# Performance work log

Measured on AMD Instinct MI355X. Metric: run time of the kernel, lower is better.

The kernel has to match this reference:

```python
import jax, jax.numpy as jnp
import numpy as np

B, S, D, H = 4, 2048, 1024, 16
HD = D // H  # head dim = 64


def setup_inputs() -> dict:
    key = jax.random.key(0)
    ks = jax.random.split(key, 6)
    hidden_states = jax.random.normal(ks[0], (B, S, D), dtype=jnp.float32)
    attention_mask = jnp.zeros((B, S), dtype=bool)  # ignored by the module (set to None in forward)
    # RoPE cache: standard rotary angles per position
    inv_freq = 1.0 / (10000.0 ** (jnp.arange(0, HD, 2, dtype=jnp.float32) / HD))  # [HD/2]
    ang = jnp.arange(S, dtype=jnp.float32)[:, None] * inv_freq[None, :]  # [S, HD/2]
    ang = jnp.concatenate([ang, ang], axis=-1)  # [S, HD]
    rope_cos = jnp.cos(ang)
    rope_sin = jnp.sin(ang)
    scale = 1.0 / np.sqrt(D)
    Wq = jax.random.normal(ks[1], (D, D), dtype=jnp.float32) * scale
    Wk = jax.random.normal(ks[2], (D, D), dtype=jnp.float32) * scale
    Wv = jax.random.normal(ks[3], (D, D), dtype=jnp.float32) * scale
    return {"hidden_states": hidden_states, "attention_mask": attention_mask,
            "rope_cos": rope_cos, "rope_sin": rope_sin, "Wq": Wq, "Wk": Wk, "Wv": Wv}


def _rotate_half(x):
    x1, x2 = jnp.split(x, 2, axis=-1)
    return jnp.concatenate([-x2, x1], axis=-1)


def _apply_rope(x, cos, sin):
    # x: [B, H, S, HD]; cos/sin: [S, HD]
    return x * cos[None, None, :, :] + _rotate_half(x) * sin[None, None, :, :]


def reference(hidden_states, attention_mask, rope_cos, rope_sin, Wq, Wk, Wv):
    del attention_mask  # forward() sets attention_mask = None
    b, s, d = hidden_states.shape
    # QKV projections (nn.Linear: y = x @ W.T), split into heads -> [B, H, S, HD]
    def proj(W):
        y = jnp.einsum('bsd,ed->bse', hidden_states, W)
        return y.reshape(b, s, H, HD).transpose(0, 2, 1, 3)
    q = _apply_rope(proj(Wq), rope_cos, rope_sin)
    k = _apply_rope(proj(Wk), rope_cos, rope_sin)
    v = proj(Wv)
    # Softmax attention (non-causal, dropout_p=0)
    scores = jnp.einsum('bhqd,bhkd->bhqk', q, k) / np.sqrt(HD)
    probs = jax.nn.softmax(scores, axis=-1)
    ctx = jnp.einsum('bhqk,bhkd->bhqd', probs, v)
    # [B, H, S, HD] -> [B, S, D]
    return ctx.transpose(0, 2, 1, 3).reshape(b, s, d)
```

## Files before the change

kernel.cpp:

```cpp
#include <hip/hip_runtime.h>
#include <hip/hip_bf16.h>
#include <stdint.h>


typedef __attribute__((ext_vector_type(4))) float    f32x4;
typedef __attribute__((ext_vector_type(8))) __bf16   bf16x8;
typedef __attribute__((ext_vector_type(8))) unsigned short ushort8;
typedef __attribute__((ext_vector_type(4))) unsigned short ushort4v;

#define QSCALE 0.18033688011112042f
#define SMAX   16.0f

#define GL16(g, l)                                                            \
  __builtin_amdgcn_global_load_lds(                                           \
      (const __attribute__((address_space(1))) void*)(g),                     \
      (__attribute__((address_space(3))) void*)(l), 16, 0, 0)

__device__ inline unsigned short bf(float f) {
  return __builtin_bit_cast(unsigned short, (__bf16)f);
}

__global__ __launch_bounds__(256) void cvt_bf16(
    const float* __restrict__ X,
    const float* __restrict__ Wq, const float* __restrict__ Wk,
    const float* __restrict__ Wv,
    unsigned short* __restrict__ Xb, unsigned short* __restrict__ Wb)
{
  const int seg = blockIdx.y;
  const float* __restrict__ src = (seg == 0) ? X : (seg == 1) ? Wq : (seg == 2) ? Wk : Wv;
  unsigned short* __restrict__ dst = (seg == 0) ? Xb : Wb + (size_t)(seg - 1) * 1048576;
  const size_t n8 = (seg == 0) ? (size_t)1048576 : (size_t)131072;
  const size_t stride = (size_t)gridDim.x * 256;
  for (size_t i = blockIdx.x * 256 + threadIdx.x; i < n8; i += stride) {
    const float4 a = *reinterpret_cast<const float4*>(src + i * 8);
    const float4 b = *reinterpret_cast<const float4*>(src + i * 8 + 4);
    ushort8 o = { bf(a.x), bf(a.y), bf(a.z), bf(a.w), bf(b.x), bf(b.y), bf(b.z), bf(b.w) };
    *reinterpret_cast<ushort8*>(dst + i * 8) = o;
  }
}

__global__ __launch_bounds__(256) void qkv_gemm(
    const unsigned short* __restrict__ Xb, const unsigned short* __restrict__ Wb,
    const float* __restrict__ rc, const float* __restrict__ rs,
    unsigned short* __restrict__ Qb, unsigned short* __restrict__ Kb,
    unsigned short* __restrict__ VbT, int col0, int nheads_c, int gx)
{
  const int nwg = gridDim.x;
  const int q8 = nwg >> 3;
  int w = (blockIdx.x % 8) * q8 + blockIdx.x / 8;
  const int z = w / (gx * 64);
  const int r = w - z * gx * 64;
  const int brow = (r / gx) * 128;
  const int bcol = (r % gx) * 128;

  const unsigned short* __restrict__ Wz = Wb + (size_t)z * 1048576;

  const int tid  = threadIdx.x;
  const int lane = tid & 63;
  const int wid  = tid >> 6;
  const int wm = wid >> 1, wn = wid & 1;
  const int col16 = lane & 15, rowg = lane >> 4;

  __shared__ unsigned short As[128 * 32];
  __shared__ unsigned short Bs[128 * 32];

  f32x4 acc[4][4];
  #pragma unroll
  for (int m = 0; m < 4; ++m)
    #pragma unroll
    for (int n = 0; n < 4; ++n) acc[m][n] = (f32x4)0.f;

  const int srow = wid * 16 + (lane >> 2);
  const int scol = (lane & 3) * 8;
  const unsigned short* gA0 = Xb + (size_t)(brow + srow) * 1024 + scol;
  const unsigned short* gA1 = gA0 + (size_t)64 * 1024;
  const unsigned short* gB0 = Wz + (size_t)(col0 + bcol + srow) * 1024 + scol;
  const unsigned short* gB1 = gB0 + (size_t)64 * 1024;
  unsigned short* lA0 = &As[wid * 16 * 32];
  unsigned short* lA1 = &As[(64 + wid * 16) * 32];
  unsigned short* lB0 = &Bs[wid * 16 * 32];
  unsigned short* lB1 = &Bs[(64 + wid * 16) * 32];

  for (int k0 = 0; k0 < 1024; k0 += 32) {
    GL16(gA0 + k0, lA0);
    GL16(gA1 + k0, lA1);
    GL16(gB0 + k0, lB0);
    GL16(gB1 + k0, lB1);
    __syncthreads();

    bf16x8 af[4], bfv[4];
    #pragma unroll
    for (int m = 0; m < 4; ++m)
      af[m] = __builtin_bit_cast(bf16x8, *reinterpret_cast<const ushort8*>(
                &As[(wm * 64 + m * 16 + col16) * 32 + rowg * 8]));
    #pragma unroll
    for (int n = 0; n < 4; ++n)
      bfv[n] = __builtin_bit_cast(bf16x8, *reinterpret_cast<const ushort8*>(
                &Bs[(wn * 64 + n * 16 + col16) * 32 + rowg * 8]));
    #pragma unroll
    for (int m = 0; m < 4; ++m)
      #pragma unroll
      for (int n = 0; n < 4; ++n)
        acc[m][n] = __builtin_amdgcn_mfma_f32_16x16x32_bf16(af[m], bfv[n], acc[m][n], 0, 0, 0);
    __syncthreads();
  }

  #pragma unroll
  for (int m = 0; m < 4; ++m) {
    #pragma unroll
    for (int n = 0; n < 4; ++n) {
      const int e  = bcol + wn * 64 + n * 16 + col16;
      const int hl = e >> 6, hd = e & 63;
      if (z == 2) {
        const int row0 = brow + wm * 64 + m * 16 + rowg * 4;
        const int b = row0 >> 11, s0 = row0 & 2047;
        ushort4v o = { bf(acc[m][n][0]), bf(acc[m][n][1]), bf(acc[m][n][2]), bf(acc[m][n][3]) };
        *reinterpret_cast<ushort4v*>(
            VbT + ((size_t)(b * nheads_c + hl) * 64 + hd) * 2048 + s0) = o;
      } else {
        unsigned short* __restrict__ outp = (z == 0) ? Qb : Kb;
        #pragma unroll
        for (int j = 0; j < 4; ++j) {
          const int row = brow + wm * 64 + m * 16 + rowg * 4 + j;
          const int b = row >> 11, s = row & 2047;
          const float rot = (n < 2) ? -acc[m][n + 2][j] : acc[m][n - 2][j];
          float v = acc[m][n][j] * rc[s * 64 + hd] + rot * rs[s * 64 + hd];
          if (z == 0) v *= QSCALE;
          outp[((size_t)(b * nheads_c + hl) * 2048 + s) * 64 + hd] = bf(v);
        }
      }
    }
  }
}

__global__ __launch_bounds__(512) void attn(
    const unsigned short* __restrict__ Qb, const unsigned short* __restrict__ Kb,
    const unsigned short* __restrict__ VbT, float* __restrict__ out,
    int col0, int nheads_c)
{
  const int tid = threadIdx.x, lane = tid & 63, wq = tid >> 6;
  const int col16 = lane & 15, rowg = lane >> 4;

  int wg = blockIdx.x;
  const int qx = (int)gridDim.x >> 3;
  wg = (wg & 7) * qx + (wg >> 3);
  const int bh = wg >> 4;
  const int q0 = (wg & 15) * 128;
  const int b = bh / nheads_c, hl = bh - b * nheads_c;
  const int hg = (col0 >> 6) + hl;
  const size_t base = (size_t)bh * 2048 * 64;

  __shared__ unsigned short Ks[64 * 72];
  __shared__ unsigned short Vt[64 * 72];
  __shared__ unsigned short Ps[128 * 76];

  const int sr = tid >> 3, sc8 = (tid & 7) * 8;

  #pragma unroll
  for (int p = 0; p < 2; ++p) {
    const int row = p * 64 + sr;
    ushort8 v = *reinterpret_cast<const ushort8*>(Qb + base + (size_t)(q0 + row) * 64 + sc8);
    *reinterpret_cast<ushort8*>(&Ps[row * 76 + sc8]) = v;
  }
  __syncthreads();
  bf16x8 qf[2];
  #pragma unroll
  for (int ks = 0; ks < 2; ++ks)
    qf[ks] = __builtin_bit_cast(bf16x8, *reinterpret_cast<const ushort8*>(
        &Ps[(wq * 16 + col16) * 76 + ks * 32 + rowg * 8]));

  float lsum[4] = {0.f, 0.f, 0.f, 0.f};
  f32x4 acc[4];
  #pragma unroll
  for (int hf = 0; hf < 4; ++hf) acc[hf] = (f32x4)0.f;

  for (int kt = 0; kt < 32; ++kt) {
    const int key0 = kt * 64;
    {
      ushort8 kv = *reinterpret_cast<const ushort8*>(Kb + base + (size_t)(key0 + sr) * 64 + sc8);
      ushort8 vv = *reinterpret_cast<const ushort8*>(VbT + base + (size_t)sr * 2048 + key0 + sc8);
      *reinterpret_cast<ushort8*>(&Ks[sr * 72 + sc8]) = kv;
      *reinterpret_cast<ushort8*>(&Vt[sr * 72 + sc8]) = vv;
    }
    __syncthreads();

    f32x4 sc[4];
    #pragma unroll
    for (int kf = 0; kf < 4; ++kf) sc[kf] = (f32x4)0.f;
    #pragma unroll
    for (int kf = 0; kf < 4; ++kf) {
      #pragma unroll
      for (int ks = 0; ks < 2; ++ks) {
        bf16x8 kfrag = __builtin_bit_cast(bf16x8, *reinterpret_cast<const ushort8*>(
            &Ks[(kf * 16 + col16) * 72 + ks * 32 + rowg * 8]));
        sc[kf] = __builtin_amdgcn_mfma_f32_16x16x32_bf16(qf[ks], kfrag, sc[kf], 0, 0, 0);
      }
    }

    #pragma unroll
    for (int j = 0; j < 4; ++j) {
      float ps = 0.f;
      #pragma unroll
      for (int kf = 0; kf < 4; ++kf) {
        const float p = __builtin_exp2f(sc[kf][j] - SMAX);
        sc[kf][j] = p;
        ps += p;
      }
      lsum[j] += ps;
    }

    #pragma unroll
    for (int kf = 0; kf < 4; ++kf)
      #pragma unroll
      for (int j = 0; j < 4; ++j)
        Ps[(wq * 16 + rowg * 4 + j) * 76 + kf * 16 + col16] = bf(sc[kf][j]);
    __syncthreads();

    #pragma unroll
    for (int ks = 0; ks < 2; ++ks) {
      bf16x8 pf = __builtin_bit_cast(bf16x8, *reinterpret_cast<const ushort8*>(
          &Ps[(wq * 16 + col16) * 76 + ks * 32 + rowg * 8]));
      #pragma unroll
      for (int hf = 0; hf < 4; ++hf) {
        bf16x8 vf = __builtin_bit_cast(bf16x8, *reinterpret_cast<const ushort8*>(
            &Vt[(hf * 16 + col16) * 72 + ks * 32 + rowg * 8]));
        acc[hf] = __builtin_amdgcn_mfma_f32_16x16x32_bf16(pf, vf, acc[hf], 0, 0, 0);
      }
    }
    __syncthreads();
  }

  #pragma unroll
  for (int j = 0; j < 4; ++j) {
    float l = lsum[j];
    l += __shfl_xor(l, 1);
    l += __shfl_xor(l, 2);
    l += __shfl_xor(l, 4);
    l += __shfl_xor(l, 8);
    const float inv = 1.0f / l;
    const int s = q0 + wq * 16 + rowg * 4 + j;
    #pragma unroll
    for (int hf = 0; hf < 4; ++hf) {
      const int hd = hf * 16 + col16;
      out[((size_t)(b * 2048 + s)) * 1024 + hg * 64 + hd] = acc[hf][j] * inv;
    }
  }
}

extern "C" void kernel_launch(void* const* d_in, const int* in_sizes, int n_in,
                              void* d_out, int out_size, void* d_ws, size_t ws_size,
                              hipStream_t stream) {
  (void)in_sizes; (void)n_in; (void)out_size;
  const float* X  = (const float*)d_in[0];
  const float* rc = (const float*)d_in[2];
  const float* rs = (const float*)d_in[3];
  const float* Wq = (const float*)d_in[4];
  const float* Wk = (const float*)d_in[5];
  const float* Wv = (const float*)d_in[6];
  float* out = (float*)d_out;

  const size_t fixed = (size_t)2 * 8192 * 1024 + (size_t)3 * 2 * 1024 * 1024;
  int NC = 8;
  for (int nc = 1; nc <= 8; nc <<= 1) {
    size_t need = (size_t)3 * 2 * 8192 * (1024 / nc) + fixed;
    if (need <= ws_size) { NC = nc; break; }
  }
  const int CW = 1024 / NC;
  const int nheads_c = CW >> 6;
  const int nBH = 4 * nheads_c;
  const int gx = CW / 128;
  const size_t pc = (size_t)8192 * CW;

  unsigned short* Qb  = (unsigned short*)d_ws;
  unsigned short* Kb  = Qb + pc;
  unsigned short* VbT = Kb + pc;
  unsigned short* Xb  = VbT + pc;
  unsigned short* Wb  = Xb + (size_t)8192 * 1024;

  cvt_bf16<<<dim3(512, 4), 256, 0, stream>>>(X, Wq, Wk, Wv, Xb, Wb);

  for (int c = 0; c < NC; ++c) {
    const int col0 = c * CW;
    qkv_gemm<<<dim3(gx * 64 * 3), 256, 0, stream>>>(
        Xb, Wb, rc, rs, Qb, Kb, VbT, col0, nheads_c, gx);
    attn<<<dim3(16 * nBH), 512, 0, stream>>>(
        Qb, Kb, VbT, out, col0, nheads_c);
  }
}
```

Baseline: 220.2 us.

## Keep softmax probabilities in registers using 32x32 MFMA and permlane swap

The attention kernel now uses 32x32x16 bf16 MFMAs with 4 waves of 256 threads, each covering 32 query rows. It computes the score tile transposed (keys by queries) so the exponentiated probabilities can be packed to bf16 with v_cvt_pk_bf16_f32. They are then rearranged into PV operand layout with permlane32_swap instead of being written to and read back from shared memory. This removes the Ps LDS buffer and one barrier per key tile, and Q fragments are loaded straight from global memory. In exchange each wave holds larger accumulators, which raises register pressure, and row sums pass through a small shared array for the final normalisation.

```diff
diff --git a/kernel.cpp b/kernel.cpp
--- a/kernel.cpp
+++ b/kernel.cpp
@@ -3,10 +3,13 @@
 #include <stdint.h>
 
 
-typedef __attribute__((ext_vector_type(4))) float    f32x4;
-typedef __attribute__((ext_vector_type(8))) __bf16   bf16x8;
-typedef __attribute__((ext_vector_type(8))) unsigned short ushort8;
-typedef __attribute__((ext_vector_type(4))) unsigned short ushort4v;
+typedef __attribute__((ext_vector_type(4)))  float    f32x4;
+typedef __attribute__((ext_vector_type(16))) float    f32x16;
+typedef __attribute__((ext_vector_type(8)))  __bf16   bf16x8;
+typedef __attribute__((ext_vector_type(8)))  unsigned short ushort8;
+typedef __attribute__((ext_vector_type(4)))  unsigned short ushort4v;
+typedef __attribute__((ext_vector_type(4)))  uint32_t uint32x4;
+typedef __attribute__((ext_vector_type(2)))  uint32_t uint32x2;
 
 #define QSCALE 0.18033688011112042f
 #define SMAX   16.0f
@@ -18,6 +21,11 @@
 
 __device__ inline unsigned short bf(float f) {
   return __builtin_bit_cast(unsigned short, (__bf16)f);
+}
+__device__ inline uint32_t cvtpk(float lo, float hi) {
+  uint32_t r;
+  asm volatile("v_cvt_pk_bf16_f32 %0, %1, %2" : "=v"(r) : "v"(lo), "v"(hi));
+  return r;
 }
 
 __global__ __launch_bounds__(256) void cvt_bf16(
@@ -133,13 +141,13 @@
   }
 }
 
-__global__ __launch_bounds__(512) void attn(
+__global__ __launch_bounds__(256) void attn(
     const unsigned short* __restrict__ Qb, const unsigned short* __restrict__ Kb,
     const unsigned short* __restrict__ VbT, float* __restrict__ out,
     int col0, int nheads_c)
 {
   const int tid = threadIdx.x, lane = tid & 63, wq = tid >> 6;
-  const int col16 = lane & 15, rowg = lane >> 4;
+  const int l31 = lane & 31, hi = lane >> 5;
 
   int wg = blockIdx.x;
   const int qx = (int)gridDim.x >> 3;
@@ -152,98 +160,85 @@
 
   __shared__ unsigned short Ks[64 * 72];
   __shared__ unsigned short Vt[64 * 72];
-  __shared__ unsigned short Ps[128 * 76];
+  __shared__ float Ls[4 * 32];
+
+  const int qrow = q0 + wq * 32 + l31;
+  bf16x8 qf[4];
+  #pragma unroll
+  for (int ds = 0; ds < 4; ++ds)
+    qf[ds] = __builtin_bit_cast(bf16x8, *reinterpret_cast<const ushort8*>(
+        Qb + base + (size_t)qrow * 64 + ds * 16 + hi * 8));
+
+  f32x16 acc0 = (f32x16)0.f, acc1 = (f32x16)0.f;
+  float ps = 0.f;
 
   const int sr = tid >> 3, sc8 = (tid & 7) * 8;
-
-  #pragma unroll
-  for (int p = 0; p < 2; ++p) {
-    const int row = p * 64 + sr;
-    ushort8 v = *reinterpret_cast<const ushort8*>(Qb + base + (size_t)(q0 + row) * 64 + sc8);
-    *reinterpret_cast<ushort8*>(&Ps[row * 76 + sc8]) = v;
-  }
-  __syncthreads();
-  bf16x8 qf[2];
-  #pragma unroll
-  for (int ks = 0; ks < 2; ++ks)
-    qf[ks] = __builtin_bit_cast(bf16x8, *reinterpret_cast<const ushort8*>(
-        &Ps[(wq * 16 + col16) * 76 + ks * 32 + rowg * 8]));
-
-  float lsum[4] = {0.f, 0.f, 0.f, 0.f};
-  f32x4 acc[4];
-  #pragma unroll
-  for (int hf = 0; hf < 4; ++hf) acc[hf] = (f32x4)0.f;
 
   for (int kt = 0; kt < 32; ++kt) {
     const int key0 = kt * 64;
     {
-      ushort8 kv = *reinterpret_cast<const ushort8*>(Kb + base + (size_t)(key0 + sr) * 64 + sc8);
-      ushort8 vv = *reinterpret_cast<const ushort8*>(VbT + base + (size_t)sr * 2048 + key0 + sc8);
-      *reinterpret_cast<ushort8*>(&Ks[sr * 72 + sc8]) = kv;
-      *reinterpret_cast<ushort8*>(&Vt[sr * 72 + sc8]) = vv;
-    }
-    __syncthreads();
-
-    f32x4 sc[4];
-    #pragma unroll
-    for (int kf = 0; kf < 4; ++kf) sc[kf] = (f32x4)0.f;
-    #pragma unroll
-    for (int kf = 0; kf < 4; ++kf) {
-      #pragma unroll
-      for (int ks = 0; ks < 2; ++ks) {
-        bf16x8 kfrag = __builtin_bit_cast(bf16x8, *reinterpret_cast<const ushort8*>(
-            &Ks[(kf * 16 + col16) * 72 + ks * 32 + rowg * 8]));
-        sc[kf] = __builtin_amdgcn_mfma_f32_16x16x32_bf16(qf[ks], kfrag, sc[kf], 0, 0, 0);
-      }
-    }
-
-    #pragma unroll
-    for (int j = 0; j < 4; ++j) {
-      float ps = 0.f;
-      #pragma unroll
-      for (int kf = 0; kf < 4; ++kf) {
-        const float p = __builtin_exp2f(sc[kf][j] - SMAX);
-        sc[kf][j] = p;
-        ps += p;
-      }
-      lsum[j] += ps;
-    }
-
-    #pragma unroll
-    for (int kf = 0; kf < 4; ++kf)
-      #pragma unroll
-      for (int j = 0; j < 4; ++j)
-        Ps[(wq * 16 + rowg * 4 + j) * 76 + kf * 16 + col16] = bf(sc[kf][j]);
-    __syncthreads();
-
-    #pragma unroll
-    for (int ks = 0; ks < 2; ++ks) {
-      bf16x8 pf = __builtin_bit_cast(bf16x8, *reinterpret_cast<const ushort8*>(
-          &Ps[(wq * 16 + col16) * 76 + ks * 32 + rowg * 8]));
-      #pragma unroll
-      for (int hf = 0; hf < 4; ++hf) {
-        bf16x8 vf = __builtin_bit_cast(bf16x8, *reinterpret_cast<const ushort8*>(
-            &Vt[(hf * 16 + col16) * 72 + ks * 32 + rowg * 8]));
-        acc[hf] = __builtin_amdgcn_mfma_f32_16x16x32_bf16(pf, vf, acc[hf], 0, 0, 0);
-      }
-    }
-    __syncthreads();
-  }
-
-  #pragma unroll
-  for (int j = 0; j < 4; ++j) {
-    float l = lsum[j];
-    l += __shfl_xor(l, 1);
-    l += __shfl_xor(l, 2);
-    l += __shfl_xor(l, 4);
-    l += __shfl_xor(l, 8);
-    const float inv = 1.0f / l;
-    const int s = q0 + wq * 16 + rowg * 4 + j;
-    #pragma unroll
-    for (int hf = 0; hf < 4; ++hf) {
-      const int hd = hf * 16 + col16;
-      out[((size_t)(b * 2048 + s)) * 1024 + hg * 64 + hd] = acc[hf][j] * inv;
-    }
+      ushort8 k0v = *reinterpret_cast<const ushort8*>(Kb + base + (size_t)(key0 + sr) * 64 + sc8);
+      ushort8 k1v = *reinterpret_cast<const ushort8*>(Kb + base + (size_t)(key0 + 32 + sr) * 64 + sc8);
+      ushort8 v0v = *reinterpret_cast<const ushort8*>(VbT + base + (size_t)sr * 2048 + key0 + sc8);
+      ushort8 v1v = *reinterpret_cast<const ushort8*>(VbT + base + (size_t)(32 + sr) * 2048 + key0 + sc8);
+      *reinterpret_cast<ushort8*>(&Ks[sr * 72 + sc8]) = k0v;
+      *reinterpret_cast<ushort8*>(&Ks[(32 + sr) * 72 + sc8]) = k1v;
+      *reinterpret_cast<ushort8*>(&Vt[sr * 72 + sc8]) = v0v;
+      *reinterpret_cast<ushort8*>(&Vt[(32 + sr) * 72 + sc8]) = v1v;
+    }
+    __syncthreads();
+
+    bf16x8 pa[4];
+    #pragma unroll
+    for (int kb = 0; kb < 2; ++kb) {
+      f32x16 s = (f32x16)0.f;
+      #pragma unroll
+      for (int ds = 0; ds < 4; ++ds) {
+        bf16x8 af = __builtin_bit_cast(bf16x8, *reinterpret_cast<const ushort8*>(
+            &Ks[(kb * 32 + l31) * 72 + ds * 16 + hi * 8]));
+        s = __builtin_amdgcn_mfma_f32_32x32x16_bf16(af, qf[ds], s, 0, 0, 0);
+      }
+      float p[16];
+      #pragma unroll
+      for (int rg = 0; rg < 16; ++rg) {
+        p[rg] = __builtin_exp2f(s[rg] - SMAX);
+        ps += p[rg];
+      }
+      #pragma unroll
+      for (int hf2 = 0; hf2 < 2; ++hf2) {
+        uint32_t w0 = cvtpk(p[hf2 * 8 + 0], p[hf2 * 8 + 1]);
+        uint32_t w1 = cvtpk(p[hf2 * 8 + 2], p[hf2 * 8 + 3]);
+        uint32_t w2 = cvtpk(p[hf2 * 8 + 4], p[hf2 * 8 + 5]);
+        uint32_t w3 = cvtpk(p[hf2 * 8 + 6], p[hf2 * 8 + 7]);
+        uint32x2 a02 = __builtin_amdgcn_permlane32_swap(w0, w2, false, false);
+        uint32x2 a13 = __builtin_amdgcn_permlane32_swap(w1, w3, false, false);
+        uint32x4 d4 = { a02[0], a13[0], a02[1], a13[1] };
+        pa[kb * 2 + hf2] = __builtin_bit_cast(bf16x8, d4);
+      }
+    }
+
+    #pragma unroll
+    for (int ks = 0; ks < 4; ++ks) {
+      bf16x8 vf0 = __builtin_bit_cast(bf16x8, *reinterpret_cast<const ushort8*>(
+          &Vt[l31 * 72 + ks * 16 + hi * 8]));
+      bf16x8 vf1 = __builtin_bit_cast(bf16x8, *reinterpret_cast<const ushort8*>(
+          &Vt[(32 + l31) * 72 + ks * 16 + hi * 8]));
+      acc0 = __builtin_amdgcn_mfma_f32_32x32x16_bf16(pa[ks], vf0, acc0, 0, 0, 0);
+      acc1 = __builtin_amdgcn_mfma_f32_32x32x16_bf16(pa[ks], vf1, acc1, 0, 0, 0);
+    }
+    __syncthreads();
+  }
+
+  ps += __shfl_xor(ps, 32);
+  if (hi == 0) Ls[wq * 32 + l31] = ps;
+  #pragma unroll
+  for (int rg = 0; rg < 16; ++rg) {
+    const int qr = (rg & 3) + 8 * (rg >> 2) + 4 * hi;
+    const float inv = 1.0f / Ls[wq * 32 + qr];
+    const int s = q0 + wq * 32 + qr;
+    float* o = out + ((size_t)(b * 2048 + s)) * 1024 + hg * 64 + l31;
+    o[0]  = acc0[rg] * inv;
+    o[32] = acc1[rg] * inv;
   }
 }
 
@@ -283,7 +278,7 @@
     const int col0 = c * CW;
     qkv_gemm<<<dim3(gx * 64 * 3), 256, 0, stream>>>(
         Xb, Wb, rc, rs, Qb, Kb, VbT, col0, nheads_c, gx);
-    attn<<<dim3(16 * nBH), 512, 0, stream>>>(
+    attn<<<dim3(16 * nBH), 256, 0, stream>>>(
         Qb, Kb, VbT, out, col0, nheads_c);
   }
 }
```

New measurement: 202.9 us. 1.09x faster.
